# Optimization experiments

Measured on AMD Instinct MI355X. Metric: run time of the kernel, lower is better.

Reference implementation:

```python
import jax, jax.numpy as jnp
import numpy as np

B, N, FIN, FOUT, H = 4, 1024, 256, 256, 8
HID = FOUT // H
ALPHA = 0.2  # LeakyReLU negative slope
NEG = -1e10  # mask fill value (matches -10000000000.0)


def setup_inputs() -> dict:
    key = jax.random.key(0)
    k1, k2, k3, k4, k5 = jax.random.split(key, 5)
    h = jax.random.normal(k1, (B, N, FIN), dtype=jnp.float32)
    adj = jax.random.randint(k2, (B, N, N), 0, 2, dtype=jnp.int32)
    W = jax.random.normal(k3, (FIN, H * HID), dtype=jnp.float32) * 0.05
    a = jax.random.normal(k4, (2 * HID,), dtype=jnp.float32) * 0.05
    bias = jax.random.normal(k5, (FOUT,), dtype=jnp.float32) * 0.05
    return {"h": h, "adj": adj, "W": W, "a": a, "bias": bias}


def reference(h, adj, W, a, bias):
    b, n = h.shape[0], h.shape[1]
    hid = W.shape[1] // H
    s = (h @ W).reshape(b, n, H, hid)  # [B,N,H,F]
    # attention(cat(s_i, s_j)) == s_i @ a_left + s_j @ a_right
    a_left, a_right = a[:hid], a[hid:]
    e_i = jnp.einsum('bnhf,f->bnh', s, a_left)   # [B,N,H]
    e_j = jnp.einsum('bnhf,f->bnh', s, a_right)  # [B,N,H]
    e = e_i[:, :, None, :] + e_j[:, None, :, :]  # [B,i,j,H]
    e = jnp.where(e > 0, e, ALPHA * e)           # LeakyReLU(0.2)
    masked = jnp.where(adj[..., None] == 0, NEG, e)
    # NOTE: original applies softmax over dim=1 (the i axis), then contracts over j
    att = jax.nn.softmax(masked, axis=1)
    # dropout omitted (eval mode / deterministic reference)
    h_prime = jnp.einsum('bijh,bjhf->bihf', att, s)
    out = h_prime.reshape(b, n, H * hid) + bias
    return out
```

## Files before the change

### kernel.cpp

```cpp
#include <hip/hip_runtime.h>
#include <hip/hip_bf16.h>

constexpr int Bb  = 4;
constexpr int Nn  = 1024;
constexpr int Fin = 256;
constexpr int Cc  = 256;
constexpr int Hh  = 8;
constexpr int Hid = 32;
constexpr float Alpha = 0.2f;
constexpr float L2E = 1.4426950408889634f;
constexpr int NCHUNK = 16;

typedef __attribute__((ext_vector_type(8))) short bf16x8;
typedef __attribute__((ext_vector_type(4))) float f32x4;

__device__ __forceinline__ unsigned cvt_pk_bf16(float lo, float hi) {
    unsigned r;
    asm("v_cvt_pk_bf16_f32 %0, %1, %2" : "=v"(r) : "v"(lo), "v"(hi));
    return r;
}

constexpr int BM = 64, BN = 64, BK = 32;

__global__ __launch_bounds__(256) void k_gemm(const float* __restrict__ hin,
                                              const float* __restrict__ W,
                                              float* __restrict__ s) {
    __shared__ float As[BM * BK];
    __shared__ float Bs[BK * BN];
    const int t = threadIdx.x;
    const int row0 = blockIdx.y * BM;
    const int col0 = blockIdx.x * BN;
    const int tx = t & 15, ty = t >> 4;
    float acc[4][4] = {};
    for (int k0 = 0; k0 < Fin; k0 += BK) {
        #pragma unroll
        for (int v = t; v < BM * BK / 4; v += 256) {
            int r = v >> 3, k4 = v & 7;
            float4 av = *reinterpret_cast<const float4*>(
                &hin[(size_t)(row0 + r) * Fin + k0 + k4 * 4]);
            *reinterpret_cast<float4*>(&As[r * 32 + ((k4 ^ (r & 7)) << 2)]) = av;
        }
        #pragma unroll
        for (int v = t; v < BK * BN / 4; v += 256) {
            int kk = v >> 4, c4 = v & 15;
            *reinterpret_cast<float4*>(&Bs[kk * BN + c4 * 4]) =
                *reinterpret_cast<const float4*>(
                    &W[(size_t)(k0 + kk) * Cc + col0 + c4 * 4]);
        }
        __syncthreads();
        #pragma unroll
        for (int kq = 0; kq < BK / 4; ++kq) {
            const int slot = (kq ^ (ty & 7)) << 2;
            float4 am[4];
            #pragma unroll
            for (int m = 0; m < 4; ++m)
                am[m] = *reinterpret_cast<const float4*>(&As[(ty + 16 * m) * 32 + slot]);
            float4 bk[4];
            #pragma unroll
            for (int kk = 0; kk < 4; ++kk)
                bk[kk] = *reinterpret_cast<const float4*>(&Bs[(kq * 4 + kk) * BN + tx * 4]);
            #pragma unroll
            for (int m = 0; m < 4; ++m) {
                acc[m][0] = fmaf(am[m].x, bk[0].x, acc[m][0]);
                acc[m][1] = fmaf(am[m].x, bk[0].y, acc[m][1]);
                acc[m][2] = fmaf(am[m].x, bk[0].z, acc[m][2]);
                acc[m][3] = fmaf(am[m].x, bk[0].w, acc[m][3]);
                acc[m][0] = fmaf(am[m].y, bk[1].x, acc[m][0]);
                acc[m][1] = fmaf(am[m].y, bk[1].y, acc[m][1]);
                acc[m][2] = fmaf(am[m].y, bk[1].z, acc[m][2]);
                acc[m][3] = fmaf(am[m].y, bk[1].w, acc[m][3]);
                acc[m][0] = fmaf(am[m].z, bk[2].x, acc[m][0]);
                acc[m][1] = fmaf(am[m].z, bk[2].y, acc[m][1]);
                acc[m][2] = fmaf(am[m].z, bk[2].z, acc[m][2]);
                acc[m][3] = fmaf(am[m].z, bk[2].w, acc[m][3]);
                acc[m][0] = fmaf(am[m].w, bk[3].x, acc[m][0]);
                acc[m][1] = fmaf(am[m].w, bk[3].y, acc[m][1]);
                acc[m][2] = fmaf(am[m].w, bk[3].z, acc[m][2]);
                acc[m][3] = fmaf(am[m].w, bk[3].w, acc[m][3]);
            }
        }
        __syncthreads();
    }
    #pragma unroll
    for (int m = 0; m < 4; ++m) {
        float4 o = make_float4(acc[m][0], acc[m][1], acc[m][2], acc[m][3]);
        *reinterpret_cast<float4*>(
            &s[(size_t)(row0 + ty + 16 * m) * Cc + col0 + tx * 4]) = o;
    }
}

__global__ void k_edge(const float* __restrict__ s, const float* __restrict__ av,
                       float* __restrict__ ei, float* __restrict__ ej) {
    const int idx = blockIdx.x * 256 + threadIdx.x;
    const int hh = idx & 7;
    const int bn = idx >> 3;
    const float* sp = &s[(size_t)bn * Cc + hh * Hid];
    float si = 0.f, sj = 0.f;
    #pragma unroll
    for (int f4 = 0; f4 < 8; ++f4) {
        float4 sv = *reinterpret_cast<const float4*>(&sp[f4 * 4]);
        float4 al = *reinterpret_cast<const float4*>(&av[f4 * 4]);
        float4 ar = *reinterpret_cast<const float4*>(&av[Hid + f4 * 4]);
        si += sv.x * al.x + sv.y * al.y + sv.z * al.z + sv.w * al.w;
        sj += sv.x * ar.x + sv.y * ar.y + sv.z * ar.z + sv.w * ar.w;
    }
    ei[idx] = si * L2E;
    ej[idx] = sj * L2E;
}

__global__ __launch_bounds__(256) void k_colsum(const float* __restrict__ ei,
                                                const float* __restrict__ ej,
                                                const int* __restrict__ adj,
                                                float* __restrict__ Zp,
                                                unsigned long long* __restrict__ adjBT) {
    const int ic = blockIdx.x;
    const int jt = blockIdx.y;
    const int b  = blockIdx.z;
    const int i0 = ic * 64;
    const int j0 = jt * 64;
    const int t = threadIdx.x;
    const int jj = t & 63;
    const int g = t >> 6;
    __shared__ float eis[64 * Hh];
    __shared__ float red[4 * 64 * Hh];
    for (int v = t; v < 64 * Hh; v += 256)
        eis[v] = ei[((size_t)b * Nn + i0) * Hh + v];
    float ejr[Hh];
    {
        float4 eA = *reinterpret_cast<const float4*>(&ej[((size_t)b * Nn + j0 + jj) * Hh]);
        float4 eB = *reinterpret_cast<const float4*>(&ej[((size_t)b * Nn + j0 + jj) * Hh + 4]);
        ejr[0] = eA.x; ejr[1] = eA.y; ejr[2] = eA.z; ejr[3] = eA.w;
        ejr[4] = eB.x; ejr[5] = eB.y; ejr[6] = eB.z; ejr[7] = eB.w;
    }
    __syncthreads();
    float z[Hh] = {};
    const int* ap = &adj[((size_t)b * Nn + i0 + g * 16) * Nn + j0 + jj];
    #pragma unroll 4
    for (int ii = 0; ii < 16; ++ii) {
        int a = ap[(size_t)ii * Nn];
        unsigned long long bal = __ballot(a != 0);
        if (jj == 0)
            adjBT[((size_t)b * 16 + jt) * Nn + (i0 + g * 16 + ii)] = bal;
        float mf = (float)(a != 0);
        const float* ep = &eis[(g * 16 + ii) * Hh];
        #pragma unroll
        for (int hh = 0; hh < Hh; ++hh) {
            float x = ep[hh] + ejr[hh];
            x = fmaxf(x, Alpha * x);
            z[hh] = fmaf(mf, exp2f(x), z[hh]);
        }
    }
    #pragma unroll
    for (int hh = 0; hh < Hh; ++hh)
        red[(g * 64 + jj) * Hh + hh] = z[hh];
    __syncthreads();
    for (int v = t; v < 64 * Hh; v += 256) {
        float sum = red[v] + red[512 + v] + red[1024 + v] + red[1536 + v];
        Zp[(size_t)ic * (Bb * Nn * Hh) + ((size_t)b * Nn + j0) * Hh + v] = sum;
    }
}

__global__ void k_ezrT(const float* __restrict__ Zp, const float* __restrict__ ei,
                       const float* __restrict__ ej,
                       float* __restrict__ eiT, float2* __restrict__ ezrT) {
    const int tid = blockIdx.x * 256 + threadIdx.x;
    const int n = tid & 1023;
    const int bh = tid >> 10;
    const int b = bh >> 3, h = bh & 7;
    const int src = (b * Nn + n) * Hh + h;
    constexpr int S = Bb * Nn * Hh;
    float sum = 0.f;
    #pragma unroll
    for (int c = 0; c < NCHUNK; ++c) sum += Zp[(size_t)c * S + src];
    ezrT[tid] = make_float2(ej[src], 1.0f / sum);
    eiT[tid] = ei[src];
}

__global__ __launch_bounds__(256) void k_pack(const float* __restrict__ s,
                                              unsigned short* __restrict__ sB) {
    const int tid = blockIdx.x * 256 + threadIdx.x;
    const int l  = tid & 63;
    const int fh = (tid >> 6) & 1;
    const int jt = (tid >> 7) & 31;
    const int bh = tid >> 12;
    const int b = bh >> 3, h = bh & 7;
    const int j = jt * 32 + (l >> 4) * 8;
    const int f = fh * 16 + (l & 15);
    const float* sp = &s[((size_t)b * Nn + j) * Cc + h * Hid + f];
    float v[8];
    #pragma unroll
    for (int e = 0; e < 8; ++e) v[e] = sp[(size_t)e * Cc];
    uint4 pk;
    pk.x = cvt_pk_bf16(v[0], v[1]);
    pk.y = cvt_pk_bf16(v[2], v[3]);
    pk.z = cvt_pk_bf16(v[4], v[5]);
    pk.w = cvt_pk_bf16(v[6], v[7]);
    *reinterpret_cast<uint4*>(&sB[(size_t)bh * 32768 + jt * 1024 + fh * 512 + l * 8]) = pk;
}

__global__ __launch_bounds__(256) void k_agg(const unsigned short* __restrict__ sB,
                                             const float* __restrict__ eiT,
                                             const float2* __restrict__ ezrT,
                                             const unsigned long long* __restrict__ adjBT,
                                             const float* __restrict__ bias,
                                             float* __restrict__ out) {
    const int bid = blockIdx.x;
    const int xcd = bid & 7, g = bid >> 3;
    const int bh = xcd * 4 + (g & 3);
    const int it = g >> 2;
    const int b = bh >> 3, h = bh & 7;
    const int t = threadIdx.x, w = t >> 6, l = t & 63;
    const int lg = l >> 4;
    const int row = it * 64 + w * 16 + (l & 15);
    const float ei_r = eiT[bh * Nn + row];

    const float4* ez4 = reinterpret_cast<const float4*>(ezrT + (size_t)bh * Nn);
    const unsigned short* sbp = sB + (size_t)bh * 32768;

    f32x4 acc0 = {0.f, 0.f, 0.f, 0.f}, acc1 = {0.f, 0.f, 0.f, 0.f};

    for (int jk = 0; jk < 32; ++jk) {
        const int j8 = jk * 32 + lg * 8;
        float4 za = ez4[(j8 >> 1) + 0];
        float4 zb = ez4[(j8 >> 1) + 1];
        float4 zc = ez4[(j8 >> 1) + 2];
        float4 zd = ez4[(j8 >> 1) + 3];
        unsigned long long m64 = adjBT[((size_t)b * 16 + (jk >> 1)) * Nn + row];
        unsigned mb = (unsigned)(m64 >> ((jk & 1) * 32 + lg * 8)) & 0xFFu;

        float wv[8];
        {
            float ejv[8] = {za.x, za.z, zb.x, zb.z, zc.x, zc.z, zd.x, zd.z};
            float rzv[8] = {za.y, za.w, zb.y, zb.w, zc.y, zc.w, zd.y, zd.w};
            #pragma unroll
            for (int e = 0; e < 8; ++e) {
                float x = ei_r + ejv[e];
                x = fmaxf(x, Alpha * x);
                float ww = exp2f(x) * rzv[e];
                wv[e] = ((mb >> e) & 1u) ? ww : 0.0f;
            }
        }
        union { bf16x8 v; unsigned u[4]; } A;
        A.u[0] = cvt_pk_bf16(wv[0], wv[1]);
        A.u[1] = cvt_pk_bf16(wv[2], wv[3]);
        A.u[2] = cvt_pk_bf16(wv[4], wv[5]);
        A.u[3] = cvt_pk_bf16(wv[6], wv[7]);

        bf16x8 b0 = *reinterpret_cast<const bf16x8*>(sbp + (size_t)jk * 1024 + l * 8);
        bf16x8 b1 = *reinterpret_cast<const bf16x8*>(sbp + (size_t)jk * 1024 + 512 + l * 8);

        acc0 = __builtin_amdgcn_mfma_f32_16x16x32_bf16(A.v, b0, acc0, 0, 0, 0);
        acc1 = __builtin_amdgcn_mfma_f32_16x16x32_bf16(A.v, b1, acc1, 0, 0, 0);
    }

    const int col = l & 15;
    const float bv0 = bias[h * Hid + col];
    const float bv1 = bias[h * Hid + 16 + col];
    const int r0 = it * 64 + w * 16 + lg * 4;
    #pragma unroll
    for (int reg = 0; reg < 4; ++reg) {
        float* op = &out[((size_t)b * Nn + r0 + reg) * Cc + h * Hid];
        op[col]      = acc0[reg] + bv0;
        op[16 + col] = acc1[reg] + bv1;
    }
}

extern "C" void kernel_launch(void* const* d_in, const int* in_sizes, int n_in,
                              void* d_out, int out_size, void* d_ws, size_t ws_size,
                              hipStream_t stream) {
    const float* hin  = (const float*)d_in[0];
    const int*   adj  = (const int*)d_in[1];
    const float* W    = (const float*)d_in[2];
    const float* a    = (const float*)d_in[3];
    const float* bias = (const float*)d_in[4];
    float* out = (float*)d_out;
    float* ws  = (float*)d_ws;

    float*  s    = ws;
    float*  ei   = ws + 1048576;
    float*  ej   = ws + 1081344;
    float*  Zp   = ws + 1114112;
    float*  eiT  = ws + 1638400;
    float2* ezrT = (float2*)(ws + 1671168);
    unsigned long long* adjBT = (unsigned long long*)(ws + 1736704);
    unsigned short* sB = (unsigned short*)(ws + 1867776);

    k_gemm  <<<dim3(Cc / BN, (Bb * Nn) / BM), 256, 0, stream>>>(hin, W, s);
    k_edge  <<<dim3((Bb * Nn * Hh) / 256),    256, 0, stream>>>(s, a, ei, ej);
    k_colsum<<<dim3(16, 16, 4),               256, 0, stream>>>(ei, ej, adj, Zp, adjBT);
    k_ezrT  <<<dim3((Bb * Nn * Hh) / 256),    256, 0, stream>>>(Zp, ei, ej, eiT, ezrT);
    k_pack  <<<dim3(512),                     256, 0, stream>>>(s, sB);
    k_agg   <<<dim3(512),                     256, 0, stream>>>(sB, eiT, ezrT, adjBT, bias, out);
}
```

Measured before the change: 132.0 us.

## Fuse projection GEMM with edge scores and bf16 packing using MFMA

Replaces the fp32 FMA projection GEMM with a bf16 MFMA GEMM that stages whole K-slabs of h and W in LDS. The epilogue computes the per-head attention logits (ei, ej) through cross-lane shuffles and writes the projected features directly in the bf16 layout the aggregation kernel consumes. This removes the k_edge and k_pack launches and the fp32 round trip of s through global memory. It also changes the ei/ej layout to head-major for colsum. The cost is that ei/ej are now computed from a bf16-input GEMM, which reduces precision, and the LDS footprint per block is larger.

```diff
diff --git a/kernel.cpp b/kernel.cpp
--- a/kernel.cpp
+++ b/kernel.cpp
@@ -20,96 +20,102 @@
     return r;
 }
 
-constexpr int BM = 64, BN = 64, BK = 32;
-
 __global__ __launch_bounds__(256) void k_gemm(const float* __restrict__ hin,
                                               const float* __restrict__ W,
-                                              float* __restrict__ s) {
-    __shared__ float As[BM * BK];
-    __shared__ float Bs[BK * BN];
+                                              const float* __restrict__ av,
+                                              float* __restrict__ eiT,
+                                              float* __restrict__ ejT,
+                                              unsigned short* __restrict__ sC) {
+    __shared__ unsigned short Asm[64 * 256];
+    __shared__ unsigned short Bsm[64 * 256];
     const int t = threadIdx.x;
-    const int row0 = blockIdx.y * BM;
-    const int col0 = blockIdx.x * BN;
-    const int tx = t & 15, ty = t >> 4;
-    float acc[4][4] = {};
-    for (int k0 = 0; k0 < Fin; k0 += BK) {
-        #pragma unroll
-        for (int v = t; v < BM * BK / 4; v += 256) {
-            int r = v >> 3, k4 = v & 7;
-            float4 av = *reinterpret_cast<const float4*>(
-                &hin[(size_t)(row0 + r) * Fin + k0 + k4 * 4]);
-            *reinterpret_cast<float4*>(&As[r * 32 + ((k4 ^ (r & 7)) << 2)]) = av;
-        }
-        #pragma unroll
-        for (int v = t; v < BK * BN / 4; v += 256) {
-            int kk = v >> 4, c4 = v & 15;
-            *reinterpret_cast<float4*>(&Bs[kk * BN + c4 * 4]) =
-                *reinterpret_cast<const float4*>(
-                    &W[(size_t)(k0 + kk) * Cc + col0 + c4 * 4]);
-        }
-        __syncthreads();
-        #pragma unroll
-        for (int kq = 0; kq < BK / 4; ++kq) {
-            const int slot = (kq ^ (ty & 7)) << 2;
-            float4 am[4];
+    const int hp = blockIdx.x;
+    const int rt = blockIdx.y;
+    const int b = rt >> 4;
+    const int row0m = (rt & 15) * 64;
+    const int grow0 = rt * 64;
+    const int col0 = hp * 64;
+
+    #pragma unroll
+    for (int i = 0; i < 16; ++i) {
+        int fi = i * 256 + t;
+        int r = fi >> 6, c4 = fi & 63;
+        float4 v = *reinterpret_cast<const float4*>(&hin[(size_t)(grow0 + r) * Fin + c4 * 4]);
+        uint2 pk = make_uint2(cvt_pk_bf16(v.x, v.y), cvt_pk_bf16(v.z, v.w));
+        *reinterpret_cast<uint2*>(reinterpret_cast<char*>(Asm) + r * 512 +
+            (((c4 >> 1) ^ ((r >> 1) & 7)) << 4) + ((c4 & 1) << 3)) = pk;
+    }
+    #pragma unroll
+    for (int i = 0; i < 32; ++i) {
+        int p = i * 256 + t;
+        int c = p & 63, k = (p >> 6) << 1;
+        float w0 = W[(size_t)k * Cc + col0 + c];
+        float w1 = W[(size_t)(k + 1) * Cc + col0 + c];
+        unsigned pk = cvt_pk_bf16(w0, w1);
+        *reinterpret_cast<unsigned*>(reinterpret_cast<char*>(Bsm) + c * 512 +
+            (((k >> 3) ^ ((c >> 1) & 7)) << 4) + ((k & 7) << 1)) = pk;
+    }
+    __syncthreads();
+
+    const int w = t >> 6, l = t & 63;
+    const int lr = l & 15, lg = l >> 4;
+    const int ar = w * 16 + lr;
+    f32x4 acc[4] = {{0.f,0.f,0.f,0.f},{0.f,0.f,0.f,0.f},{0.f,0.f,0.f,0.f},{0.f,0.f,0.f,0.f}};
+
+    #pragma unroll
+    for (int ks = 0; ks < 8; ++ks) {
+        bf16x8 af = *reinterpret_cast<const bf16x8*>(reinterpret_cast<char*>(Asm) +
+            ar * 512 + ((((ks << 2) + lg) ^ ((ar >> 1) & 7)) << 4));
+        #pragma unroll
+        for (int n = 0; n < 4; ++n) {
+            int c = n * 16 + lr;
+            bf16x8 bf = *reinterpret_cast<const bf16x8*>(reinterpret_cast<char*>(Bsm) +
+                c * 512 + ((((ks << 2) + lg) ^ ((c >> 1) & 7)) << 4));
+            acc[n] = __builtin_amdgcn_mfma_f32_16x16x32_bf16(af, bf, acc[n], 0, 0, 0);
+        }
+    }
+
+    const int jt16 = (row0m >> 4) + w;
+    #pragma unroll
+    for (int n = 0; n < 4; ++n) {
+        int bh = b * 8 + hp * 2 + (n >> 1);
+        uint2 pk = make_uint2(cvt_pk_bf16(acc[n][0], acc[n][1]),
+                              cvt_pk_bf16(acc[n][2], acc[n][3]));
+        *reinterpret_cast<uint2*>(reinterpret_cast<char*>(sC) +
+            ((((size_t)bh * 64 + jt16) * 2 + (n & 1)) * 64 + l) * 8) = pk;
+    }
+
+    float aL0 = av[lr], aL1 = av[16 + lr], aR0 = av[32 + lr], aR1 = av[48 + lr];
+    #pragma unroll
+    for (int hh = 0; hh < 2; ++hh) {
+        float pi[4], pj[4];
+        #pragma unroll
+        for (int reg = 0; reg < 4; ++reg) {
+            pi[reg] = acc[hh * 2][reg] * aL0 + acc[hh * 2 + 1][reg] * aL1;
+            pj[reg] = acc[hh * 2][reg] * aR0 + acc[hh * 2 + 1][reg] * aR1;
+        }
+        #pragma unroll
+        for (int m = 1; m < 16; m <<= 1) {
             #pragma unroll
-            for (int m = 0; m < 4; ++m)
-                am[m] = *reinterpret_cast<const float4*>(&As[(ty + 16 * m) * 32 + slot]);
-            float4 bk[4];
+            for (int reg = 0; reg < 4; ++reg) {
+                pi[reg] += __shfl_xor(pi[reg], m);
+                pj[reg] += __shfl_xor(pj[reg], m);
+            }
+        }
+        if (lr == 0) {
+            int bh = b * 8 + hp * 2 + hh;
             #pragma unroll
-            for (int kk = 0; kk < 4; ++kk)
-                bk[kk] = *reinterpret_cast<const float4*>(&Bs[(kq * 4 + kk) * BN + tx * 4]);
-            #pragma unroll
-            for (int m = 0; m < 4; ++m) {
-                acc[m][0] = fmaf(am[m].x, bk[0].x, acc[m][0]);
-                acc[m][1] = fmaf(am[m].x, bk[0].y, acc[m][1]);
-                acc[m][2] = fmaf(am[m].x, bk[0].z, acc[m][2]);
-                acc[m][3] = fmaf(am[m].x, bk[0].w, acc[m][3]);
-                acc[m][0] = fmaf(am[m].y, bk[1].x, acc[m][0]);
-                acc[m][1] = fmaf(am[m].y, bk[1].y, acc[m][1]);
-                acc[m][2] = fmaf(am[m].y, bk[1].z, acc[m][2]);
-                acc[m][3] = fmaf(am[m].y, bk[1].w, acc[m][3]);
-                acc[m][0] = fmaf(am[m].z, bk[2].x, acc[m][0]);
-                acc[m][1] = fmaf(am[m].z, bk[2].y, acc[m][1]);
-                acc[m][2] = fmaf(am[m].z, bk[2].z, acc[m][2]);
-                acc[m][3] = fmaf(am[m].z, bk[2].w, acc[m][3]);
-                acc[m][0] = fmaf(am[m].w, bk[3].x, acc[m][0]);
-                acc[m][1] = fmaf(am[m].w, bk[3].y, acc[m][1]);
-                acc[m][2] = fmaf(am[m].w, bk[3].z, acc[m][2]);
-                acc[m][3] = fmaf(am[m].w, bk[3].w, acc[m][3]);
+            for (int reg = 0; reg < 4; ++reg) {
+                int row = row0m + w * 16 + lg * 4 + reg;
+                eiT[bh * Nn + row] = pi[reg] * L2E;
+                ejT[bh * Nn + row] = pj[reg] * L2E;
             }
         }
-        __syncthreads();
-    }
-    #pragma unroll
-    for (int m = 0; m < 4; ++m) {
-        float4 o = make_float4(acc[m][0], acc[m][1], acc[m][2], acc[m][3]);
-        *reinterpret_cast<float4*>(
-            &s[(size_t)(row0 + ty + 16 * m) * Cc + col0 + tx * 4]) = o;
-    }
-}
-
-__global__ void k_edge(const float* __restrict__ s, const float* __restrict__ av,
-                       float* __restrict__ ei, float* __restrict__ ej) {
-    const int idx = blockIdx.x * 256 + threadIdx.x;
-    const int hh = idx & 7;
-    const int bn = idx >> 3;
-    const float* sp = &s[(size_t)bn * Cc + hh * Hid];
-    float si = 0.f, sj = 0.f;
-    #pragma unroll
-    for (int f4 = 0; f4 < 8; ++f4) {
-        float4 sv = *reinterpret_cast<const float4*>(&sp[f4 * 4]);
-        float4 al = *reinterpret_cast<const float4*>(&av[f4 * 4]);
-        float4 ar = *reinterpret_cast<const float4*>(&av[Hid + f4 * 4]);
-        si += sv.x * al.x + sv.y * al.y + sv.z * al.z + sv.w * al.w;
-        sj += sv.x * ar.x + sv.y * ar.y + sv.z * ar.z + sv.w * ar.w;
-    }
-    ei[idx] = si * L2E;
-    ej[idx] = sj * L2E;
-}
-
-__global__ __launch_bounds__(256) void k_colsum(const float* __restrict__ ei,
-                                                const float* __restrict__ ej,
+    }
+}
+
+__global__ __launch_bounds__(256) void k_colsum(const float* __restrict__ eiT,
+                                                const float* __restrict__ ejT,
                                                 const int* __restrict__ adj,
                                                 float* __restrict__ Zp,
                                                 unsigned long long* __restrict__ adjBT) {
@@ -123,15 +129,14 @@
     const int g = t >> 6;
     __shared__ float eis[64 * Hh];
     __shared__ float red[4 * 64 * Hh];
-    for (int v = t; v < 64 * Hh; v += 256)
-        eis[v] = ei[((size_t)b * Nn + i0) * Hh + v];
+    for (int v = t; v < 64 * Hh; v += 256) {
+        int h = v >> 6, i = v & 63;
+        eis[i * Hh + h] = eiT[((size_t)b * Hh + h) * Nn + i0 + i];
+    }
     float ejr[Hh];
-    {
-        float4 eA = *reinterpret_cast<const float4*>(&ej[((size_t)b * Nn + j0 + jj) * Hh]);
-        float4 eB = *reinterpret_cast<const float4*>(&ej[((size_t)b * Nn + j0 + jj) * Hh + 4]);
-        ejr[0] = eA.x; ejr[1] = eA.y; ejr[2] = eA.z; ejr[3] = eA.w;
-        ejr[4] = eB.x; ejr[5] = eB.y; ejr[6] = eB.z; ejr[7] = eB.w;
-    }
+    #pragma unroll
+    for (int hh = 0; hh < Hh; ++hh)
+        ejr[hh] = ejT[((size_t)b * Hh + hh) * Nn + j0 + jj];
     __syncthreads();
     float z[Hh] = {};
     const int* ap = &adj[((size_t)b * Nn + i0 + g * 16) * Nn + j0 + jj];
@@ -160,9 +165,8 @@
     }
 }
 
-__global__ void k_ezrT(const float* __restrict__ Zp, const float* __restrict__ ei,
-                       const float* __restrict__ ej,
-                       float* __restrict__ eiT, float2* __restrict__ ezrT) {
+__global__ void k_ezrT(const float* __restrict__ Zp, const float* __restrict__ ejT,
+                       float2* __restrict__ ezrT) {
     const int tid = blockIdx.x * 256 + threadIdx.x;
     const int n = tid & 1023;
     const int bh = tid >> 10;
@@ -172,33 +176,10 @@
     float sum = 0.f;
     #pragma unroll
     for (int c = 0; c < NCHUNK; ++c) sum += Zp[(size_t)c * S + src];
-    ezrT[tid] = make_float2(ej[src], 1.0f / sum);
-    eiT[tid] = ei[src];
-}
-
-__global__ __launch_bounds__(256) void k_pack(const float* __restrict__ s,
-                                              unsigned short* __restrict__ sB) {
-    const int tid = blockIdx.x * 256 + threadIdx.x;
-    const int l  = tid & 63;
-    const int fh = (tid >> 6) & 1;
-    const int jt = (tid >> 7) & 31;
-    const int bh = tid >> 12;
-    const int b = bh >> 3, h = bh & 7;
-    const int j = jt * 32 + (l >> 4) * 8;
-    const int f = fh * 16 + (l & 15);
-    const float* sp = &s[((size_t)b * Nn + j) * Cc + h * Hid + f];
-    float v[8];
-    #pragma unroll
-    for (int e = 0; e < 8; ++e) v[e] = sp[(size_t)e * Cc];
-    uint4 pk;
-    pk.x = cvt_pk_bf16(v[0], v[1]);
-    pk.y = cvt_pk_bf16(v[2], v[3]);
-    pk.z = cvt_pk_bf16(v[4], v[5]);
-    pk.w = cvt_pk_bf16(v[6], v[7]);
-    *reinterpret_cast<uint4*>(&sB[(size_t)bh * 32768 + jt * 1024 + fh * 512 + l * 8]) = pk;
-}
-
-__global__ __launch_bounds__(256) void k_agg(const unsigned short* __restrict__ sB,
+    ezrT[tid] = make_float2(ejT[tid], 1.0f / sum);
+}
+
+__global__ __launch_bounds__(256) void k_agg(const unsigned short* __restrict__ sC,
                                              const float* __restrict__ eiT,
                                              const float2* __restrict__ ezrT,
                                              const unsigned long long* __restrict__ adjBT,
@@ -215,7 +196,9 @@
     const float ei_r = eiT[bh * Nn + row];
 
     const float4* ez4 = reinterpret_cast<const float4*>(ezrT + (size_t)bh * Nn);
-    const unsigned short* sbp = sB + (size_t)bh * 32768;
+    const unsigned long long* scp =
+        reinterpret_cast<const unsigned long long*>(sC) + (size_t)bh * 8192;
+    const int lpos = ((l >> 4) & 1) * 32 + (l & 15);
 
     f32x4 acc0 = {0.f, 0.f, 0.f, 0.f}, acc1 = {0.f, 0.f, 0.f, 0.f};
 
@@ -246,11 +229,15 @@
         A.u[2] = cvt_pk_bf16(wv[4], wv[5]);
         A.u[3] = cvt_pk_bf16(wv[6], wv[7]);
 
-        bf16x8 b0 = *reinterpret_cast<const bf16x8*>(sbp + (size_t)jk * 1024 + l * 8);
-        bf16x8 b1 = *reinterpret_cast<const bf16x8*>(sbp + (size_t)jk * 1024 + 512 + l * 8);
-
-        acc0 = __builtin_amdgcn_mfma_f32_16x16x32_bf16(A.v, b0, acc0, 0, 0, 0);
-        acc1 = __builtin_amdgcn_mfma_f32_16x16x32_bf16(A.v, b1, acc1, 0, 0, 0);
+        const int j16 = jk * 2 + (l >> 5);
+        union { bf16x8 v; unsigned long long q[2]; } B0, B1;
+        const unsigned long long* p0 = scp + ((size_t)j16 * 2 + 0) * 64 + lpos;
+        const unsigned long long* p1 = scp + ((size_t)j16 * 2 + 1) * 64 + lpos;
+        B0.q[0] = p0[0];  B0.q[1] = p0[16];
+        B1.q[0] = p1[0];  B1.q[1] = p1[16];
+
+        acc0 = __builtin_amdgcn_mfma_f32_16x16x32_bf16(A.v, B0.v, acc0, 0, 0, 0);
+        acc1 = __builtin_amdgcn_mfma_f32_16x16x32_bf16(A.v, B1.v, acc1, 0, 0, 0);
     }
 
     const int col = l & 15;
@@ -276,19 +263,15 @@
     float* out = (float*)d_out;
     float* ws  = (float*)d_ws;
 
-    float*  s    = ws;
-    float*  ei   = ws + 1048576;
-    float*  ej   = ws + 1081344;
-    float*  Zp   = ws + 1114112;
-    float*  eiT  = ws + 1638400;
-    float2* ezrT = (float2*)(ws + 1671168);
-    unsigned long long* adjBT = (unsigned long long*)(ws + 1736704);
-    unsigned short* sB = (unsigned short*)(ws + 1867776);
-
-    k_gemm  <<<dim3(Cc / BN, (Bb * Nn) / BM), 256, 0, stream>>>(hin, W, s);
-    k_edge  <<<dim3((Bb * Nn * Hh) / 256),    256, 0, stream>>>(s, a, ei, ej);
-    k_colsum<<<dim3(16, 16, 4),               256, 0, stream>>>(ei, ej, adj, Zp, adjBT);
-    k_ezrT  <<<dim3((Bb * Nn * Hh) / 256),    256, 0, stream>>>(Zp, ei, ej, eiT, ezrT);
-    k_pack  <<<dim3(512),                     256, 0, stream>>>(s, sB);
-    k_agg   <<<dim3(512),                     256, 0, stream>>>(sB, eiT, ezrT, adjBT, bias, out);
-}
+    float*  eiT  = ws;
+    float*  ejT  = ws + 32768;
+    float*  Zp   = ws + 65536;
+    float2* ezrT = (float2*)(ws + 589824);
+    unsigned long long* adjBT = (unsigned long long*)(ws + 655360);
+    unsigned short* sC = (unsigned short*)(ws + 786432);
+
+    k_gemm  <<<dim3(4, 64),                 256, 0, stream>>>(hin, W, a, eiT, ejT, sC);
+    k_colsum<<<dim3(16, 16, 4),             256, 0, stream>>>(eiT, ejT, adj, Zp, adjBT);
+    k_ezrT  <<<dim3((Bb * Nn * Hh) / 256),  256, 0, stream>>>(Zp, ejT, ezrT);
+    k_agg   <<<dim3(512),                   256, 0, stream>>>(sC, eiT, ezrT, adjBT, bias, out);
+}
```

New measurement: 115.3 us. -12.6%, faster.
